# Optimization experiments

Measured on AMD Instinct MI355X. Metric: run time of the kernel, lower is better.

The kernel has to match this reference:

```python
import jax, jax.numpy as jnp
import numpy as np

DIM_PN = 64
N_P = 16
BN_EPS = 1e-5


def _conv1x1(h, w, b):
    # h: (B, Cin, N), w: (Cout, Cin), b: (Cout,)
    return jnp.einsum('oc,bcn->bon', w, h) + b[None, :, None]


def _bn(h, g, be):
    # training-mode BatchNorm1d: stats over (batch, points)
    m = h.mean(axis=(0, 2), keepdims=True)
    v = h.var(axis=(0, 2), keepdims=True)
    return (h - m) * jax.lax.rsqrt(v + BN_EPS) * g[None, :, None] + be[None, :, None]


def setup_inputs() -> dict:
    key = jax.random.key(0)
    ks = jax.random.split(key, 8)
    B, N = 32, 16384
    x = jax.random.normal(ks[0], (B, 3, N), dtype=jnp.float32)
    def kaiming(k, shape):
        fan_in = shape[1]
        return jax.random.normal(k, shape, dtype=jnp.float32) * np.float32(1.0 / np.sqrt(fan_in))
    w1 = kaiming(ks[1], (64, 3));   b1 = jnp.zeros((64,), jnp.float32)
    w2 = kaiming(ks[2], (128, 64)); b2 = jnp.zeros((128,), jnp.float32)
    w3 = kaiming(ks[3], (DIM_PN, 128)); b3 = jnp.zeros((DIM_PN,), jnp.float32)
    g1 = jnp.ones((64,), jnp.float32); be1 = jnp.zeros((64,), jnp.float32)
    g2 = jnp.ones((128,), jnp.float32); be2 = jnp.zeros((128,), jnp.float32)
    g3 = jnp.ones((DIM_PN,), jnp.float32); be3 = jnp.zeros((DIM_PN,), jnp.float32)
    return {"x": x, "w1": w1, "b1": b1, "g1": g1, "be1": be1,
            "w2": w2, "b2": b2, "g2": g2, "be2": be2,
            "w3": w3, "b3": b3, "g3": g3, "be3": be3}


def reference(x, w1, b1, g1, be1, w2, b2, g2, be2, w3, b3, g3, be3):
    # SoftPoolfeat forward (core of MSN), vectorized SoftPool.
    h = jax.nn.relu(_bn(_conv1x1(x, w1, b1), g1, be1))       # (B,64,N)
    h = jax.nn.relu(_bn(_conv1x1(h, w2, b2), g2, be2))       # (B,128,N)
    h = _bn(_conv1x1(h, w3, b3), g3, be3)                    # (B,C=64,N)
    # SoftPool: per channel c, ascending sort order over points, keep first N_p.
    idx = jnp.argsort(h, axis=2)[:, :, :N_P]                 # (B,C,Np) int32
    # sp_cube[b, c2, c, n] = h[b, c2, idx[b, c, n]]
    sp_cube = jnp.take_along_axis(h[:, :, None, :], idx[:, None, :, :], axis=3)  # (B,C,C,Np)
    # partial[b, ch, c, n] = x[b, ch, idx[b, c, n]]  (original repeats x over featdim then gathers)
    partial = jnp.take_along_axis(x[:, :, None, :], idx[:, None, :, :], axis=3)  # (B,3,C,Np)
    feat = jnp.concatenate([partial, sp_cube], axis=1)       # (B,3+C,C,Np)
    sp_idx = jnp.broadcast_to(idx[:, None, :, :], (idx.shape[0], 3, idx.shape[1], idx.shape[2]))
    return feat, sp_idx
```

## Files before the change

### kernel.cpp

```cpp
#include <hip/hip_runtime.h>
#include <cstddef>

#pragma clang fp contract(off)

#define B_    32
#define N_    16384
#define NPTS  (B_ * N_)
#define FEATSZ (32 * 67 * 64 * 16)
#define NCHUNK (NPTS / 64)
#define GRID_Y2 1024
#define GRID_XS 512

enum : int {
  D_X9    = 0,
  D_Y3SUM = 16,
  D_Y3SQ  = 80,
  D_Y2S   = 144,
  D_Y2Q   = 272,
  D_XPART = 1024,
};
enum : int {
  F_M1   = 16384,
  F_R1   = 16448,
  F_M2   = 16512,
  F_R2   = 16640,
  F_M3   = 16768,
  F_R3   = 16832,
  F_W2T  = 16896,
  F_W3T  = 25088,
  F_TOPK = 33280,
};
#define Y3_B     524288
#define Y2PART_B 524288

__device__ __forceinline__ float h1_of(const float* __restrict__ w1,
                                       const float* __restrict__ b1,
                                       const float* __restrict__ g1,
                                       const float* __restrict__ be1,
                                       const float* __restrict__ fw, int c,
                                       float x0, float x1, float x2) {
  float s = w1[c*3+0] * x0;
  s = fmaf(w1[c*3+1], x1, s);
  s = fmaf(w1[c*3+2], x2, s);
  float y1 = s + b1[c];
  float t = y1 - fw[F_M1 + c];
  float u = t * fw[F_R1 + c];
  u = u * g1[c];
  u = u + be1[c];
  return fmaxf(u, 0.f);
}

__device__ __forceinline__ unsigned int okey(float f) {
  unsigned int u = __float_as_uint(f);
  return (u & 0x80000000u) ? ~u : (u | 0x80000000u);
}

__global__ __launch_bounds__(256) void k_xstats64(const float* __restrict__ x,
                                                  double* __restrict__ wd) {
  __shared__ double sacc[4][9];
  double a0=0,a1=0,a2=0,m00=0,m01=0,m02=0,m11=0,m12=0,m22=0;
  for (int p = blockIdx.x * 256 + threadIdx.x; p < NPTS; p += gridDim.x * 256) {
    int b = p >> 14, n = p & (N_ - 1);
    const float* xb = x + (size_t)b * 3 * N_ + n;
    double x0 = xb[0], x1 = xb[N_], x2 = xb[2 * N_];
    a0 += x0; a1 += x1; a2 += x2;
    m00 = fma(x0,x0,m00); m01 = fma(x0,x1,m01); m02 = fma(x0,x2,m02);
    m11 = fma(x1,x1,m11); m12 = fma(x1,x2,m12); m22 = fma(x2,x2,m22);
  }
  #pragma unroll
  for (int m = 32; m >= 1; m >>= 1) {
    a0 += __shfl_xor(a0, m); a1 += __shfl_xor(a1, m); a2 += __shfl_xor(a2, m);
    m00 += __shfl_xor(m00, m); m01 += __shfl_xor(m01, m); m02 += __shfl_xor(m02, m);
    m11 += __shfl_xor(m11, m); m12 += __shfl_xor(m12, m); m22 += __shfl_xor(m22, m);
  }
  const int wv = threadIdx.x >> 6;
  if ((threadIdx.x & 63) == 0) {
    sacc[wv][0] = a0;  sacc[wv][1] = a1;  sacc[wv][2] = a2;
    sacc[wv][3] = m00; sacc[wv][4] = m01; sacc[wv][5] = m02;
    sacc[wv][6] = m11; sacc[wv][7] = m12; sacc[wv][8] = m22;
  }
  __syncthreads();
  if (threadIdx.x < 9) {
    double s = ((sacc[0][threadIdx.x] + sacc[1][threadIdx.x])
              + sacc[2][threadIdx.x]) + sacc[3][threadIdx.x];
    wd[D_XPART + blockIdx.x * 9 + threadIdx.x] = s;
  }
}

__global__ __launch_bounds__(64) void k_redX(double* __restrict__ wd) {
  int j = threadIdx.x;
  if (j >= 9) return;
  double s = 0.0;
  for (int b = 0; b < GRID_XS; ++b) s += wd[D_XPART + b * 9 + j];
  wd[D_X9 + j] = s;
}

__global__ void k_prep1(const float* __restrict__ w1, const float* __restrict__ b1,
                        double* __restrict__ wd, float* __restrict__ fw) {
  int c = threadIdx.x;
  if (c >= 64) return;
  const double inv = 1.0 / (double)NPTS;
  double mx0 = wd[0]*inv, mx1 = wd[1]*inv, mx2 = wd[2]*inv;
  double c00 = wd[3]*inv - mx0*mx0, c01 = wd[4]*inv - mx0*mx1, c02 = wd[5]*inv - mx0*mx2;
  double c11 = wd[6]*inv - mx1*mx1, c12 = wd[7]*inv - mx1*mx2, c22 = wd[8]*inv - mx2*mx2;
  double w0 = w1[c*3+0], w1_ = w1[c*3+1], w2_ = w1[c*3+2];
  double m1 = w0*mx0 + w1_*mx1 + w2_*mx2 + (double)b1[c];
  double var = w0*w0*c00 + w1_*w1_*c11 + w2_*w2_*c22
             + 2.0*(w0*w1_*c01 + w0*w2_*c02 + w1_*w2_*c12);
  fw[F_M1 + c] = (float)m1;
  float vpe = (float)var + 1e-5f;
  fw[F_R1 + c] = (float)(1.0 / sqrt((double)vpe));
}

__global__ __launch_bounds__(64) void k_prepW(const float* __restrict__ w2,
                                              const float* __restrict__ w3,
                                              float* __restrict__ fw) {
  const int o = blockIdx.x, c = threadIdx.x;
  fw[F_W2T + c * 128 + o] = w2[o * 64 + c];
  fw[F_W3T + o * 64 + c] = w3[c * 128 + o];
}

__global__ __launch_bounds__(1024, 8) void k_y2stats(const float* __restrict__ x,
                                                     const float* __restrict__ w1,
                                                     const float* __restrict__ b1,
                                                     const float* __restrict__ g1,
                                                     const float* __restrict__ be1,
                                                     const float* __restrict__ fw,
                                                     double* __restrict__ y2part) {
  __shared__ float h1g[16][64][4];
  const int tid = threadIdx.x;
  const int lane = tid & 63;
  const int wvu = __builtin_amdgcn_readfirstlane(tid >> 6);
  const int o0 = wvu * 8;
  const float* w2t = fw + F_W2T;
  double s64[8], q64[8];
  #pragma unroll
  for (int j = 0; j < 8; ++j) { s64[j] = 0.0; q64[j] = 0.0; }

  for (int chunk = blockIdx.x; chunk < NCHUNK; chunk += GRID_Y2) {
    __syncthreads();
    {
      int p = chunk * 64 + lane;
      int b = p >> 14, n = p & (N_ - 1);
      const float* xb = x + (size_t)b * 3 * N_ + n;
      float x0 = xb[0], x1 = xb[N_], x2 = xb[2 * N_];
      const int c0 = wvu * 4;
      float hv[4];
      #pragma unroll
      for (int k = 0; k < 4; ++k) hv[k] = h1_of(w1, b1, g1, be1, fw, c0 + k, x0, x1, x2);
      float4 v; v.x = hv[0]; v.y = hv[1]; v.z = hv[2]; v.w = hv[3];
      *(float4*)&h1g[wvu][lane][0] = v;
    }
    __syncthreads();
    float acc[8];
    #pragma unroll
    for (int j = 0; j < 8; ++j) acc[j] = 0.f;
    #pragma unroll 4
    for (int cg = 0; cg < 16; ++cg) {
      float4 hgv = *(const float4*)&h1g[cg][lane][0];
      float hx[4] = {hgv.x, hgv.y, hgv.z, hgv.w};
      #pragma unroll
      for (int e = 0; e < 4; ++e) {
        const int c = cg * 4 + e;
        const float hc = hx[e];
        const float* wc = w2t + c * 128 + o0;
        #pragma unroll
        for (int j = 0; j < 8; ++j) acc[j] = fmaf(wc[j], hc, acc[j]);
      }
    }
    #pragma unroll
    for (int j = 0; j < 8; ++j) {
      double v = (double)acc[j];
      s64[j] += v;
      q64[j] = fma(v, v, q64[j]);
    }
  }
  #pragma unroll
  for (int j = 0; j < 8; ++j) {
    #pragma unroll
    for (int m = 32; m >= 1; m >>= 1) {
      s64[j] += __shfl_xor(s64[j], m);
      q64[j] += __shfl_xor(q64[j], m);
    }
  }
  if (lane == 0) {
    #pragma unroll
    for (int j = 0; j < 8; ++j) {
      int o = o0 + j;
      y2part[((size_t)blockIdx.x * 128 + o) * 2 + 0] = s64[j];
      y2part[((size_t)blockIdx.x * 128 + o) * 2 + 1] = q64[j];
    }
  }
}

__global__ __launch_bounds__(256) void k_redY2(const double* __restrict__ y2part,
                                               double* __restrict__ wd) {
  __shared__ double ss[256], sq[256];
  const int o = blockIdx.x, tid = threadIdx.x;
  double s = 0.0, q = 0.0;
  for (int blk = tid; blk < GRID_Y2; blk += 256) {
    s += y2part[((size_t)blk * 128 + o) * 2 + 0];
    q += y2part[((size_t)blk * 128 + o) * 2 + 1];
  }
  ss[tid] = s; sq[tid] = q;
  __syncthreads();
  for (int st = 128; st > 0; st >>= 1) {
    if (tid < st) { ss[tid] += ss[tid + st]; sq[tid] += sq[tid + st]; }
    __syncthreads();
  }
  if (tid == 0) { wd[D_Y2S + o] = ss[0]; wd[D_Y2Q + o] = sq[0]; }
}

__global__ void k_prep2s(const float* __restrict__ b2,
                         double* __restrict__ wd, float* __restrict__ fw) {
  int o = threadIdx.x;
  if (o >= 128) return;
  const double inv = 1.0 / (double)NPTS;
  double mraw = wd[D_Y2S + o] * inv;
  double var = wd[D_Y2Q + o] * inv - mraw * mraw;
  fw[F_M2 + o] = (float)(mraw + (double)b2[o]);
  float vpe = (float)var + 1e-5f;
  fw[F_R2 + o] = (float)(1.0 / sqrt((double)vpe));
}

__global__ __launch_bounds__(512, 4) void k_fwd(const float* __restrict__ x,
                                                const float* __restrict__ w1,
                                                const float* __restrict__ b1,
                                                const float* __restrict__ g1,
                                                const float* __restrict__ be1,
                                                const float* __restrict__ b2,
                                                const float* __restrict__ g2,
                                                const float* __restrict__ be2,
                                                const float* __restrict__ b3,
                                                const float* __restrict__ fw,
                                                float* __restrict__ y3out,
                                                int pbase) {
  __shared__ float h1g[16][64][4];
  __shared__ float h2g[16][64][4];
  const int tid = threadIdx.x;
  const int lane = tid & 63;
  const int wvu = __builtin_amdgcn_readfirstlane(tid >> 6);
  const int p = pbase + blockIdx.x * 64 + lane;
  const int b = p >> 14, n = p & (N_ - 1);
  const float* xb = x + (size_t)b * 3 * N_ + n;
  const float x0 = xb[0], x1 = xb[N_], x2 = xb[2 * N_];
  const float* w2t = fw + F_W2T;
  const float* w3t = fw + F_W3T;
  const int q0 = wvu * 8;
  float a3[8];

  {
    const int c0 = wvu * 8;
    float hv[8];
    #pragma unroll
    for (int k = 0; k < 8; ++k) hv[k] = h1_of(w1, b1, g1, be1, fw, c0 + k, x0, x1, x2);
    #pragma unroll
    for (int gq = 0; gq < 2; ++gq) {
      float4 v; v.x = hv[gq*4+0]; v.y = hv[gq*4+1]; v.z = hv[gq*4+2]; v.w = hv[gq*4+3];
      *(float4*)&h1g[(c0 >> 2) + gq][lane][0] = v;
    }
  }
  __syncthreads();

  #pragma unroll
  for (int H = 0; H < 2; ++H) {
    {
      const int o0 = H * 64 + wvu * 8;
      float acc[8];
      #pragma unroll
      for (int j = 0; j < 8; ++j) acc[j] = 0.f;
      #pragma unroll 4
      for (int cg = 0; cg < 16; ++cg) {
        float4 hgv = *(const float4*)&h1g[cg][lane][0];
        float hx[4] = {hgv.x, hgv.y, hgv.z, hgv.w};
        #pragma unroll
        for (int e = 0; e < 4; ++e) {
          const int c = cg * 4 + e;
          const float hc = hx[e];
          const float* wc = w2t + c * 128 + o0;
          #pragma unroll
          for (int j = 0; j < 8; ++j) acc[j] = fmaf(wc[j], hc, acc[j]);
        }
      }
      float hv2[8];
      #pragma unroll
      for (int j = 0; j < 8; ++j) {
        int o = o0 + j;
        float y2 = acc[j] + b2[o];
        float t = y2 - fw[F_M2 + o];
        float u = t * fw[F_R2 + o];
        u = u * g2[o];
        u = u + be2[o];
        hv2[j] = fmaxf(u, 0.f);
      }
      #pragma unroll
      for (int gq = 0; gq < 2; ++gq) {
        float4 v; v.x = hv2[gq*4+0]; v.y = hv2[gq*4+1]; v.z = hv2[gq*4+2]; v.w = hv2[gq*4+3];
        *(float4*)&h2g[wvu * 2 + gq][lane][0] = v;
      }
    }
    __syncthreads();
    {
      #pragma unroll 4
      for (int og = 0; og < 16; ++og) {
        float4 hgv = *(const float4*)&h2g[og][lane][0];
        float hx[4] = {hgv.x, hgv.y, hgv.z, hgv.w};
        #pragma unroll
        for (int e = 0; e < 4; ++e) {
          const int o = H * 64 + og * 4 + e;
          const float ho = hx[e];
          const float* wr = w3t + o * 64 + q0;
          if (H == 0 && og == 0 && e == 0) {
            #pragma unroll
            for (int j = 0; j < 8; ++j) a3[j] = wr[j] * ho;
          } else {
            #pragma unroll
            for (int j = 0; j < 8; ++j) a3[j] = fmaf(wr[j], ho, a3[j]);
          }
        }
      }
    }
    __syncthreads();
  }

  float* yrow = y3out + (size_t)b * 64 * N_ + n;
  #pragma unroll
  for (int j = 0; j < 8; ++j) {
    int q = q0 + j;
    yrow[(size_t)q * N_] = a3[j] + b3[q];
  }
}

__global__ void k_prep3(double* __restrict__ wd, float* __restrict__ fw) {
  int o = threadIdx.x;
  if (o >= 64) return;
  const double inv = 1.0 / (double)NPTS;
  double m = wd[D_Y3SUM + o] * inv;
  double var = wd[D_Y3SQ + o] * inv - m * m;
  fw[F_M3 + o] = (float)m;
  float vpe = (float)var + 1e-5f;
  fw[F_R3 + o] = (float)(1.0 / sqrt((double)vpe));
}

__global__ __launch_bounds__(256) void k_topk(const float* __restrict__ y3,
                                              const float* __restrict__ g3,
                                              int* __restrict__ topk,
                                              double* __restrict__ wd) {
  __shared__ unsigned int hist[4][256];
  __shared__ unsigned int cnt[256];
  __shared__ unsigned long long buf[256];
  __shared__ unsigned int nbuf;
  __shared__ int s_tbin1, s_before1, s_tbin2;
  __shared__ double ssum[256], ssq[256];
  const int tid = threadIdx.x;
  const int row = blockIdx.x;
  const int c = row & 63;
  const int wv = tid >> 6;
  const float sgn = (g3[c] >= 0.f) ? 1.f : -1.f;
  const float4* y = (const float4*)(y3 + (size_t)row * N_);

  for (int i = tid; i < 1024; i += 256) ((unsigned int*)hist)[i] = 0;
  if (tid == 0) nbuf = 0;
  __syncthreads();

  double s = 0.0, q = 0.0;
  #pragma unroll 1
  for (int it = 0; it < 16; ++it) {
    int n4 = it * 256 + tid;
    float4 v = y[n4];
    {
      double a = v.x, bb = v.y, cc2 = v.z, d = v.w;
      s += a + bb + cc2 + d;
      q = fma(a,a,q); q = fma(bb,bb,q); q = fma(cc2,cc2,q); q = fma(d,d,q);
    }
    unsigned int u0 = okey(sgn * v.x), u1 = okey(sgn * v.y);
    unsigned int u2 = okey(sgn * v.z), u3 = okey(sgn * v.w);
    atomicAdd(&hist[wv][u0 >> 24], 1u);
    atomicAdd(&hist[wv][u1 >> 24], 1u);
    atomicAdd(&hist[wv][u2 >> 24], 1u);
    atomicAdd(&hist[wv][u3 >> 24], 1u);
  }
  ssum[tid] = s; ssq[tid] = q;
  __syncthreads();
  for (int st = 128; st > 0; st >>= 1) {
    if (tid < st) { ssum[tid] += ssum[tid + st]; ssq[tid] += ssq[tid + st]; }
    __syncthreads();
  }
  if (tid == 0) {
    atomicAdd(&wd[D_Y3SUM + c], ssum[0]);
    atomicAdd(&wd[D_Y3SQ  + c], ssq[0]);
  }

  unsigned int myc = hist[0][tid] + hist[1][tid] + hist[2][tid] + hist[3][tid];
  cnt[tid] = myc;
  __syncthreads();
  for (int st = 1; st < 256; st <<= 1) {
    unsigned int t = (tid >= st) ? cnt[tid - st] : 0u;
    __syncthreads();
    cnt[tid] += t;
    __syncthreads();
  }
  {
    unsigned int incl = cnt[tid], excl = incl - myc;
    if (excl < 16u && incl >= 16u) { s_tbin1 = tid; s_before1 = (int)excl; }
  }
  __syncthreads();
  const unsigned int tbin1 = (unsigned int)s_tbin1;
  const int before1 = s_before1;

  for (int i = tid; i < 1024; i += 256) ((unsigned int*)hist)[i] = 0;
  __syncthreads();
  #pragma unroll 1
  for (int it = 0; it < 16; ++it) {
    int n4 = it * 256 + tid;
    float4 v = y[n4];
    unsigned int u0 = okey(sgn * v.x), u1 = okey(sgn * v.y);
    unsigned int u2 = okey(sgn * v.z), u3 = okey(sgn * v.w);
    if ((u0 >> 24) == tbin1) atomicAdd(&hist[wv][(u0 >> 16) & 255u], 1u);
    if ((u1 >> 24) == tbin1) atomicAdd(&hist[wv][(u1 >> 16) & 255u], 1u);
    if ((u2 >> 24) == tbin1) atomicAdd(&hist[wv][(u2 >> 16) & 255u], 1u);
    if ((u3 >> 24) == tbin1) atomicAdd(&hist[wv][(u3 >> 16) & 255u], 1u);
  }
  __syncthreads();
  myc = hist[0][tid] + hist[1][tid] + hist[2][tid] + hist[3][tid];
  cnt[tid] = myc;
  __syncthreads();
  for (int st = 1; st < 256; st <<= 1) {
    unsigned int t = (tid >= st) ? cnt[tid - st] : 0u;
    __syncthreads();
    cnt[tid] += t;
    __syncthreads();
  }
  {
    const unsigned int r2 = (unsigned int)(16 - before1);
    unsigned int incl = cnt[tid], excl = incl - myc;
    if (excl < r2 && incl >= r2) s_tbin2 = tid;
  }
  __syncthreads();
  const unsigned int thresh16 = (tbin1 << 8) | (unsigned int)s_tbin2;

  #pragma unroll 1
  for (int it = 0; it < 16; ++it) {
    int n4 = it * 256 + tid;
    float4 v = y[n4];
    int nb = n4 * 4;
    unsigned int uu[4] = { okey(sgn * v.x), okey(sgn * v.y),
                           okey(sgn * v.z), okey(sgn * v.w) };
    #pragma unroll
    for (int j = 0; j < 4; ++j) {
      if ((uu[j] >> 16) <= thresh16) {
        unsigned int slot = atomicAdd(&nbuf, 1u);
        if (slot < 256u)
          buf[slot] = ((unsigned long long)uu[j] << 32) | (unsigned int)(nb + j);
      }
    }
  }
  __syncthreads();

  if (tid < 64) {
    const unsigned int m = nbuf < 256u ? nbuf : 256u;
    const unsigned long long MAXK = ~0ull;
    unsigned long long k0 = (tid +   0u) < m ? buf[tid +   0] : MAXK;
    unsigned long long k1 = (tid +  64u) < m ? buf[tid +  64] : MAXK;
    unsigned long long k2 = (tid + 128u) < m ? buf[tid + 128] : MAXK;
    unsigned long long k3 = (tid + 192u) < m ? buf[tid + 192] : MAXK;
    #pragma unroll 1
    for (int r = 0; r < 16; ++r) {
      unsigned long long a = k0 < k1 ? k0 : k1;
      unsigned long long b = k2 < k3 ? k2 : k3;
      unsigned long long kmin = a < b ? a : b;
      #pragma unroll
      for (int m2 = 32; m2 >= 1; m2 >>= 1) {
        unsigned long long o = __shfl_xor(kmin, m2);
        kmin = o < kmin ? o : kmin;
      }
      bool have = (k0 == kmin) | (k1 == kmin) | (k2 == kmin) | (k3 == kmin);
      unsigned long long bal = __ballot(have);
      int wlane = __ffsll((unsigned long long)bal) - 1;
      if (tid == wlane) {
        if (k0 == kmin) k0 = MAXK;
        else if (k1 == kmin) k1 = MAXK;
        else if (k2 == kmin) k2 = MAXK;
        else k3 = MAXK;
      }
      if (tid == 0) topk[row * 16 + r] = (int)(kmin & 0xFFFFFFFFull);
    }
  }
}

__global__ __launch_bounds__(256) void k_gather(const float* __restrict__ x,
                                                const float* __restrict__ fw,
                                                const float* __restrict__ g3,
                                                const float* __restrict__ be3,
                                                const float* __restrict__ y3,
                                                const int* __restrict__ topk,
                                                float* __restrict__ out) {
  __shared__ int s_i[16];
  __shared__ float s_m[64], s_r[64], s_g[64], s_b[64];
  const int tid = threadIdx.x;
  const int row = blockIdx.x;
  const int b = row >> 6, c = row & 63;
  if (tid < 16) s_i[tid] = topk[row * 16 + tid];
  if (tid < 64) {
    s_m[tid] = fw[F_M3 + tid]; s_r[tid] = fw[F_R3 + tid];
    s_g[tid] = g3[tid];        s_b[tid] = be3[tid];
  }
  __syncthreads();
  for (int t = tid; t < 67 * 16; t += 256) {
    int ch = t >> 4, n = t & 15, i = s_i[n];
    float v;
    if (ch < 3) {
      v = x[((size_t)b * 3 + ch) * N_ + i];
    } else {
      int c2 = ch - 3;
      float yv = y3[((size_t)b * 64 + c2) * N_ + i];
      float tt = yv - s_m[c2];
      float u = tt * s_r[c2];
      u = u * s_g[c2];
      v = u + s_b[c2];
    }
    out[(((size_t)b * 67 + ch) * 64 + c) * 16 + n] = v;
  }
  if (tid < 48) {
    int ch = tid >> 4, n = tid & 15;
    out[FEATSZ + (((size_t)b * 3 + ch) * 64 + c) * 16 + n] = (float)s_i[n];
  }
}

extern "C" void kernel_launch(void* const* d_in, const int* in_sizes, int n_in,
                              void* d_out, int out_size, void* d_ws, size_t ws_size,
                              hipStream_t stream) {
  const float* x   = (const float*)d_in[0];
  const float* w1  = (const float*)d_in[1];
  const float* b1  = (const float*)d_in[2];
  const float* g1  = (const float*)d_in[3];
  const float* be1 = (const float*)d_in[4];
  const float* w2  = (const float*)d_in[5];
  const float* b2  = (const float*)d_in[6];
  const float* g2  = (const float*)d_in[7];
  const float* be2 = (const float*)d_in[8];
  const float* w3  = (const float*)d_in[9];
  const float* b3  = (const float*)d_in[10];
  const float* g3  = (const float*)d_in[11];
  const float* be3 = (const float*)d_in[12];
  double* wd = (double*)d_ws;
  float*  fw = (float*)d_ws;
  float*  out = (float*)d_out;
  int* topk = (int*)(fw + F_TOPK);
  double* y2part = (double*)((char*)d_ws + Y2PART_B);
  float*  y3     = (float*)((char*)d_ws + Y3_B);

  hipMemsetAsync(d_ws, 0, 1152, stream);
  k_xstats64<<<GRID_XS, 256, 0, stream>>>(x, wd);
  k_redX    <<<1, 64, 0, stream>>>(wd);
  k_prep1   <<<1, 64, 0, stream>>>(w1, b1, wd, fw);
  k_prepW   <<<128, 64, 0, stream>>>(w2, w3, fw);
  k_y2stats <<<GRID_Y2, 1024, 0, stream>>>(x, w1, b1, g1, be1, fw, y2part);
  k_redY2   <<<128, 256, 0, stream>>>(y2part, wd);
  k_prep2s  <<<1, 128, 0, stream>>>(b2, wd, fw);
  k_fwd     <<<NPTS / 128, 512, 0, stream>>>(x, w1, b1, g1, be1, b2, g2, be2, b3, fw, y3, 0);
  k_fwd     <<<NPTS / 128, 512, 0, stream>>>(x, w1, b1, g1, be1, b2, g2, be2, b3, fw, y3, NPTS / 2);
  k_topk    <<<B_ * 64, 256, 0, stream>>>(y3, g3, topk, wd);
  k_prep3   <<<1, 64, 0, stream>>>(wd, fw);
  k_gather  <<<B_ * 64, 256, 0, stream>>>(x, fw, g3, be3, y3, topk, out);
  (void)in_sizes; (void)n_in; (void)out_size; (void)ws_size;
}
```

Baseline: 503.8 us.

## Prefetch next chunk's x in y2stats/fwd, merge fwd launches and fuse BN2 prep

k_y2stats and k_fwd now load the next chunk's input coordinates while the current chunk's layer-2/3 FMAs run, which hides global load latency. k_fwd now loops over two 64-point chunks per block, so the two half-grid launches become a single launch. The k_prep2s finalization moves into the Y2 reduction kernel, removing another launch. Together these drop two launches and add some register pressure in kernels with tight launch bounds.

```diff
diff --git a/kernel.cpp b/kernel.cpp
--- a/kernel.cpp
+++ b/kernel.cpp
@@ -15,8 +15,6 @@
   D_X9    = 0,
   D_Y3SUM = 16,
   D_Y3SQ  = 80,
-  D_Y2S   = 144,
-  D_Y2Q   = 272,
   D_XPART = 1024,
 };
 enum : int {
@@ -137,21 +135,35 @@
   #pragma unroll
   for (int j = 0; j < 8; ++j) { s64[j] = 0.0; q64[j] = 0.0; }
 
+  float px0, px1, px2;
+  {
+    int p = blockIdx.x * 64 + lane;
+    int b = p >> 14, n = p & (N_ - 1);
+    const float* xb = x + (size_t)b * 3 * N_ + n;
+    px0 = xb[0]; px1 = xb[N_]; px2 = xb[2 * N_];
+  }
+
   for (int chunk = blockIdx.x; chunk < NCHUNK; chunk += GRID_Y2) {
     __syncthreads();
     {
-      int p = chunk * 64 + lane;
-      int b = p >> 14, n = p & (N_ - 1);
-      const float* xb = x + (size_t)b * 3 * N_ + n;
-      float x0 = xb[0], x1 = xb[N_], x2 = xb[2 * N_];
       const int c0 = wvu * 4;
       float hv[4];
       #pragma unroll
-      for (int k = 0; k < 4; ++k) hv[k] = h1_of(w1, b1, g1, be1, fw, c0 + k, x0, x1, x2);
+      for (int k = 0; k < 4; ++k) hv[k] = h1_of(w1, b1, g1, be1, fw, c0 + k, px0, px1, px2);
       float4 v; v.x = hv[0]; v.y = hv[1]; v.z = hv[2]; v.w = hv[3];
       *(float4*)&h1g[wvu][lane][0] = v;
     }
     __syncthreads();
+    float nx0 = 0.f, nx1 = 0.f, nx2 = 0.f;
+    {
+      int nchunk = chunk + GRID_Y2;
+      if (nchunk < NCHUNK) {
+        int p = nchunk * 64 + lane;
+        int b = p >> 14, n = p & (N_ - 1);
+        const float* xb = x + (size_t)b * 3 * N_ + n;
+        nx0 = xb[0]; nx1 = xb[N_]; nx2 = xb[2 * N_];
+      }
+    }
     float acc[8];
     #pragma unroll
     for (int j = 0; j < 8; ++j) acc[j] = 0.f;
@@ -174,6 +186,7 @@
       s64[j] += v;
       q64[j] = fma(v, v, q64[j]);
     }
+    px0 = nx0; px1 = nx1; px2 = nx2;
   }
   #pragma unroll
   for (int j = 0; j < 8; ++j) {
@@ -193,8 +206,9 @@
   }
 }
 
-__global__ __launch_bounds__(256) void k_redY2(const double* __restrict__ y2part,
-                                               double* __restrict__ wd) {
+__global__ __launch_bounds__(256) void k_redY2p(const double* __restrict__ y2part,
+                                                const float* __restrict__ b2,
+                                                float* __restrict__ fw) {
   __shared__ double ss[256], sq[256];
   const int o = blockIdx.x, tid = threadIdx.x;
   double s = 0.0, q = 0.0;
@@ -208,19 +222,14 @@
     if (tid < st) { ss[tid] += ss[tid + st]; sq[tid] += sq[tid + st]; }
     __syncthreads();
   }
-  if (tid == 0) { wd[D_Y2S + o] = ss[0]; wd[D_Y2Q + o] = sq[0]; }
-}
-
-__global__ void k_prep2s(const float* __restrict__ b2,
-                         double* __restrict__ wd, float* __restrict__ fw) {
-  int o = threadIdx.x;
-  if (o >= 128) return;
-  const double inv = 1.0 / (double)NPTS;
-  double mraw = wd[D_Y2S + o] * inv;
-  double var = wd[D_Y2Q + o] * inv - mraw * mraw;
-  fw[F_M2 + o] = (float)(mraw + (double)b2[o]);
-  float vpe = (float)var + 1e-5f;
-  fw[F_R2 + o] = (float)(1.0 / sqrt((double)vpe));
+  if (tid == 0) {
+    const double inv = 1.0 / (double)NPTS;
+    double mraw = ss[0] * inv;
+    double var = sq[0] * inv - mraw * mraw;
+    fw[F_M2 + o] = (float)(mraw + (double)b2[o]);
+    float vpe = (float)var + 1e-5f;
+    fw[F_R2 + o] = (float)(1.0 / sqrt((double)vpe));
+  }
 }
 
 __global__ __launch_bounds__(512, 4) void k_fwd(const float* __restrict__ x,
@@ -233,101 +242,117 @@
                                                 const float* __restrict__ be2,
                                                 const float* __restrict__ b3,
                                                 const float* __restrict__ fw,
-                                                float* __restrict__ y3out,
-                                                int pbase) {
+                                                float* __restrict__ y3out) {
   __shared__ float h1g[16][64][4];
   __shared__ float h2g[16][64][4];
   const int tid = threadIdx.x;
   const int lane = tid & 63;
   const int wvu = __builtin_amdgcn_readfirstlane(tid >> 6);
-  const int p = pbase + blockIdx.x * 64 + lane;
-  const int b = p >> 14, n = p & (N_ - 1);
-  const float* xb = x + (size_t)b * 3 * N_ + n;
-  const float x0 = xb[0], x1 = xb[N_], x2 = xb[2 * N_];
   const float* w2t = fw + F_W2T;
   const float* w3t = fw + F_W3T;
   const int q0 = wvu * 8;
-  float a3[8];
-
+
+  float px0, px1, px2;
   {
-    const int c0 = wvu * 8;
-    float hv[8];
-    #pragma unroll
-    for (int k = 0; k < 8; ++k) hv[k] = h1_of(w1, b1, g1, be1, fw, c0 + k, x0, x1, x2);
-    #pragma unroll
-    for (int gq = 0; gq < 2; ++gq) {
-      float4 v; v.x = hv[gq*4+0]; v.y = hv[gq*4+1]; v.z = hv[gq*4+2]; v.w = hv[gq*4+3];
-      *(float4*)&h1g[(c0 >> 2) + gq][lane][0] = v;
-    }
-  }
-  __syncthreads();
-
-  #pragma unroll
-  for (int H = 0; H < 2; ++H) {
+    int p = blockIdx.x * 128 + lane;
+    int b = p >> 14, n = p & (N_ - 1);
+    const float* xb = x + (size_t)b * 3 * N_ + n;
+    px0 = xb[0]; px1 = xb[N_]; px2 = xb[2 * N_];
+  }
+
+  #pragma unroll 1
+  for (int it = 0; it < 2; ++it) {
+    const int p = blockIdx.x * 128 + it * 64 + lane;
+    const int b = p >> 14, n = p & (N_ - 1);
+    float a3[8];
+
     {
-      const int o0 = H * 64 + wvu * 8;
-      float acc[8];
+      const int c0 = wvu * 8;
+      float hv[8];
       #pragma unroll
-      for (int j = 0; j < 8; ++j) acc[j] = 0.f;
-      #pragma unroll 4
-      for (int cg = 0; cg < 16; ++cg) {
-        float4 hgv = *(const float4*)&h1g[cg][lane][0];
-        float hx[4] = {hgv.x, hgv.y, hgv.z, hgv.w};
-        #pragma unroll
-        for (int e = 0; e < 4; ++e) {
-          const int c = cg * 4 + e;
-          const float hc = hx[e];
-          const float* wc = w2t + c * 128 + o0;
-          #pragma unroll
-          for (int j = 0; j < 8; ++j) acc[j] = fmaf(wc[j], hc, acc[j]);
-        }
-      }
-      float hv2[8];
-      #pragma unroll
-      for (int j = 0; j < 8; ++j) {
-        int o = o0 + j;
-        float y2 = acc[j] + b2[o];
-        float t = y2 - fw[F_M2 + o];
-        float u = t * fw[F_R2 + o];
-        u = u * g2[o];
-        u = u + be2[o];
-        hv2[j] = fmaxf(u, 0.f);
-      }
+      for (int k = 0; k < 8; ++k) hv[k] = h1_of(w1, b1, g1, be1, fw, c0 + k, px0, px1, px2);
       #pragma unroll
       for (int gq = 0; gq < 2; ++gq) {
-        float4 v; v.x = hv2[gq*4+0]; v.y = hv2[gq*4+1]; v.z = hv2[gq*4+2]; v.w = hv2[gq*4+3];
-        *(float4*)&h2g[wvu * 2 + gq][lane][0] = v;
-      }
-    }
-    __syncthreads();
-    {
-      #pragma unroll 4
-      for (int og = 0; og < 16; ++og) {
-        float4 hgv = *(const float4*)&h2g[og][lane][0];
-        float hx[4] = {hgv.x, hgv.y, hgv.z, hgv.w};
+        float4 v; v.x = hv[gq*4+0]; v.y = hv[gq*4+1]; v.z = hv[gq*4+2]; v.w = hv[gq*4+3];
+        *(float4*)&h1g[(c0 >> 2) + gq][lane][0] = v;
+      }
+    }
+    __syncthreads();
+
+    if (it == 0) {
+      int p2 = blockIdx.x * 128 + 64 + lane;
+      int b2_ = p2 >> 14, n2 = p2 & (N_ - 1);
+      const float* xb = x + (size_t)b2_ * 3 * N_ + n2;
+      px0 = xb[0]; px1 = xb[N_]; px2 = xb[2 * N_];
+    }
+
+    #pragma unroll
+    for (int H = 0; H < 2; ++H) {
+      {
+        const int o0 = H * 64 + wvu * 8;
+        float acc[8];
         #pragma unroll
-        for (int e = 0; e < 4; ++e) {
-          const int o = H * 64 + og * 4 + e;
-          const float ho = hx[e];
-          const float* wr = w3t + o * 64 + q0;
-          if (H == 0 && og == 0 && e == 0) {
+        for (int j = 0; j < 8; ++j) acc[j] = 0.f;
+        #pragma unroll 4
+        for (int cg = 0; cg < 16; ++cg) {
+          float4 hgv = *(const float4*)&h1g[cg][lane][0];
+          float hx[4] = {hgv.x, hgv.y, hgv.z, hgv.w};
+          #pragma unroll
+          for (int e = 0; e < 4; ++e) {
+            const int c = cg * 4 + e;
+            const float hc = hx[e];
+            const float* wc = w2t + c * 128 + o0;
             #pragma unroll
-            for (int j = 0; j < 8; ++j) a3[j] = wr[j] * ho;
-          } else {
-            #pragma unroll
-            for (int j = 0; j < 8; ++j) a3[j] = fmaf(wr[j], ho, a3[j]);
+            for (int j = 0; j < 8; ++j) acc[j] = fmaf(wc[j], hc, acc[j]);
           }
         }
-      }
-    }
-    __syncthreads();
-  }
-
-  float* yrow = y3out + (size_t)b * 64 * N_ + n;
-  #pragma unroll
-  for (int j = 0; j < 8; ++j) {
-    int q = q0 + j;
-    yrow[(size_t)q * N_] = a3[j] + b3[q];
+        float hv2[8];
+        #pragma unroll
+        for (int j = 0; j < 8; ++j) {
+          int o = o0 + j;
+          float y2 = acc[j] + b2[o];
+          float t = y2 - fw[F_M2 + o];
+          float u = t * fw[F_R2 + o];
+          u = u * g2[o];
+          u = u + be2[o];
+          hv2[j] = fmaxf(u, 0.f);
+        }
+        #pragma unroll
+        for (int gq = 0; gq < 2; ++gq) {
+          float4 v; v.x = hv2[gq*4+0]; v.y = hv2[gq*4+1]; v.z = hv2[gq*4+2]; v.w = hv2[gq*4+3];
+          *(float4*)&h2g[wvu * 2 + gq][lane][0] = v;
+        }
+      }
+      __syncthreads();
+      {
+        #pragma unroll 4
+        for (int og = 0; og < 16; ++og) {
+          float4 hgv = *(const float4*)&h2g[og][lane][0];
+          float hx[4] = {hgv.x, hgv.y, hgv.z, hgv.w};
+          #pragma unroll
+          for (int e = 0; e < 4; ++e) {
+            const int o = H * 64 + og * 4 + e;
+            const float ho = hx[e];
+            const float* wr = w3t + o * 64 + q0;
+            if (H == 0 && og == 0 && e == 0) {
+              #pragma unroll
+              for (int j = 0; j < 8; ++j) a3[j] = wr[j] * ho;
+            } else {
+              #pragma unroll
+              for (int j = 0; j < 8; ++j) a3[j] = fmaf(wr[j], ho, a3[j]);
+            }
+          }
+        }
+      }
+      __syncthreads();
+    }
+
+    float* yrow = y3out + (size_t)b * 64 * N_ + n;
+    #pragma unroll
+    for (int j = 0; j < 8; ++j) {
+      int q = q0 + j;
+      yrow[(size_t)q * N_] = a3[j] + b3[q];
+    }
   }
 }
 
@@ -556,10 +581,8 @@
   k_prep1   <<<1, 64, 0, stream>>>(w1, b1, wd, fw);
   k_prepW   <<<128, 64, 0, stream>>>(w2, w3, fw);
   k_y2stats <<<GRID_Y2, 1024, 0, stream>>>(x, w1, b1, g1, be1, fw, y2part);
-  k_redY2   <<<128, 256, 0, stream>>>(y2part, wd);
-  k_prep2s  <<<1, 128, 0, stream>>>(b2, wd, fw);
-  k_fwd     <<<NPTS / 128, 512, 0, stream>>>(x, w1, b1, g1, be1, b2, g2, be2, b3, fw, y3, 0);
-  k_fwd     <<<NPTS / 128, 512, 0, stream>>>(x, w1, b1, g1, be1, b2, g2, be2, b3, fw, y3, NPTS / 2);
+  k_redY2p  <<<128, 256, 0, stream>>>(y2part, b2, fw);
+  k_fwd     <<<NPTS / 128, 512, 0, stream>>>(x, w1, b1, g1, be1, b2, g2, be2, b3, fw, y3);
   k_topk    <<<B_ * 64, 256, 0, stream>>>(y3, g3, topk, wd);
   k_prep3   <<<1, 64, 0, stream>>>(wd, fw);
   k_gather  <<<B_ * 64, 256, 0, stream>>>(x, fw, g3, be3, y3, topk, out);
```

New measurement: 508.3 us. Within noise of the previous version (+0.9%).
